# Kernel tuning notes

Hardware: AMD Instinct MI355X
Metric: run time of the kernel (lower is better)

The kernel has to match this reference:

```python
import jax, jax.numpy as jnp
import numpy as np

D_MODEL = 1024
N_HEADS = 16
D_K = D_MODEL // N_HEADS
THETA = 10000.0
SEQ = 2048
BATCH = 2


def setup_inputs() -> dict:
    key = jax.random.key(0)
    ks = jax.random.split(key, 5)
    std = (2.0 / (D_MODEL + D_MODEL)) ** 0.5
    return {
        "x": jax.random.normal(ks[0], (BATCH, SEQ, D_MODEL), dtype=jnp.float32),
        "token_positions": jnp.arange(SEQ, dtype=jnp.int64 if jax.config.jax_enable_x64 else jnp.int32),
        "wq": jax.random.normal(ks[1], (D_MODEL, D_MODEL), dtype=jnp.float32) * std,
        "wk": jax.random.normal(ks[2], (D_MODEL, D_MODEL), dtype=jnp.float32) * std,
        "wv": jax.random.normal(ks[3], (D_MODEL, D_MODEL), dtype=jnp.float32) * std,
        "wo": jax.random.normal(ks[4], (D_MODEL, D_MODEL), dtype=jnp.float32) * std,
    }


def _apply_rope(t, token_positions):
    # t: [b, h, s, d_k]; interleaved even/odd rotation (RoPE)
    k = jnp.arange(D_K // 2, dtype=t.dtype)
    inv_freq = THETA ** (-2.0 * k / D_K)                     # [d_k/2]
    angles = token_positions.astype(t.dtype)[:, None] * inv_freq  # [s, d_k/2]
    cos, sin = jnp.cos(angles), jnp.sin(angles)
    even, odd = t[..., 0::2], t[..., 1::2]
    re = even * cos - odd * sin
    ro = odd * cos + even * sin
    # re-interleave: stack last then reshape back to [..., d_k]
    return jnp.stack([re, ro], axis=-1).reshape(t.shape)


def reference(x, token_positions, wq, wk, wv, wo):
    b, s, _ = x.shape
    def proj(w):
        y = jnp.einsum("bsd,ed->bse", x, w)               # Linear: x @ W^T
        return y.reshape(b, s, N_HEADS, D_K).transpose(0, 2, 1, 3)  # [b,h,s,dk]
    q, k, v = proj(wq), proj(wk), proj(wv)
    q = _apply_rope(q, token_positions)
    k = _apply_rope(k, token_positions)
    scores = jnp.einsum("bhqd,bhkd->bhqk", q, k) / jnp.sqrt(jnp.asarray(D_K, x.dtype))
    attn = jax.nn.softmax(scores, axis=-1)
    out = jnp.einsum("bhqk,bhkd->bhqd", attn, v)          # [b,h,s,dk]
    out = out.transpose(0, 2, 1, 3).reshape(b, s, D_MODEL)
    return jnp.einsum("bsd,ed->bse", out, wo)
```

## Files before the change

kernel.cpp:

```cpp
#include <hip/hip_runtime.h>
#include <stdint.h>

typedef __bf16 bf16x8 __attribute__((ext_vector_type(8)));
typedef __bf16 bf16x2 __attribute__((ext_vector_type(2)));
typedef float f32x4 __attribute__((ext_vector_type(4)));
typedef unsigned short ushort_t;
typedef unsigned int uint;

#define SEQ    2048
#define DMODEL 1024
#define NHEAD  16
#define DKH    64
#define NBATCH 2
#define MROWS  (NBATCH*SEQ)
#define LOG2E  1.44269504088896340736f

__device__ __forceinline__ uint pk2(float a, float b) {
  bf16x2 t; t[0] = (__bf16)a; t[1] = (__bf16)b;
  return __builtin_bit_cast(uint, t);
}
__device__ __forceinline__ ushort_t b1(float a) {
  return __builtin_bit_cast(ushort_t, (__bf16)a);
}
__device__ __forceinline__ float fexp2(float x) {
#if __has_builtin(__builtin_amdgcn_exp2f)
  return __builtin_amdgcn_exp2f(x);
#else
  return exp2f(x);
#endif
}

__device__ __forceinline__ void gload16(const void* g, void* l) {
  __builtin_amdgcn_global_load_lds(
      (const __attribute__((address_space(1))) void*)g,
      (__attribute__((address_space(3))) void*)l, 16, 0, 0);
}

__device__ __forceinline__ f32x4 mfma16(bf16x8 a, bf16x8 b, f32x4 c) {
  return __builtin_amdgcn_mfma_f32_16x16x32_bf16(a, b, c, 0, 0, 0);
}

__global__ __launch_bounds__(256) void cvt_all(
    const float* __restrict__ x, const float* __restrict__ wq,
    const float* __restrict__ wk, const float* __restrict__ wv,
    const float* __restrict__ wo, uint2* __restrict__ out)
{
  int b = blockIdx.x;
  const float4* src; uint2* dst; int i;
  if (b < 4096) {
    i = b * 256 + threadIdx.x; src = (const float4*)x; dst = out;
  } else {
    int s = (b - 4096) >> 10;
    i = ((b - 4096) & 1023) * 256 + threadIdx.x;
    src = (const float4*)(s == 0 ? wq : s == 1 ? wk : s == 2 ? wv : wo);
    dst = out + (size_t)1048576 + (size_t)s * 262144;
  }
  float4 v = src[i];
  uint2 r; r.x = pk2(v.x, v.y); r.y = pk2(v.z, v.w);
  dst[i] = r;
}

__global__ __launch_bounds__(256) void rope_tab_kernel(const int* __restrict__ tokpos, float2* __restrict__ tab) {
  int t = blockIdx.x * 256 + threadIdx.x;
  int s = t >> 5, k = t & 31;
  double inv = pow(10000.0, -(double)(2 * k) / 64.0);
  double ang = (double)tokpos[s] * inv;
  tab[t] = make_float2((float)cos(ang), (float)sin(ang));
}

__global__ __launch_bounds__(256) void gemm_nt(
    const ushort_t* __restrict__ A, const ushort_t* __restrict__ W,
    const float2* __restrict__ tab,
    ushort_t* __restrict__ Qo, ushort_t* __restrict__ Ko, ushort_t* __restrict__ Vo,
    float* __restrict__ outf, int fused)
{
  __shared__ ushort_t lA[2][128 * 64];
  __shared__ ushort_t lB[2][128 * 64];
  const int tid = threadIdx.x;
  const int w = tid >> 6, l = tid & 63, lo = l & 15, hi = l >> 4;
  const int wr = (w >> 1) * 64, wc = (w & 1) * 64;
  const char* Ab = (const char*)A + (size_t)blockIdx.y * 128 * 2048;
  const char* Bb = (const char*)W + (size_t)blockIdx.x * 128 * 2048;
  f32x4 acc[4][4] = {};

  const int o0 = w * 1024 + l * 16;
  const int r0 = o0 >> 7;
  const int us = ((o0 >> 4) & 7) ^ (r0 & 7);
  const char* ap = Ab + (size_t)r0 * 2048 + us * 16;
  const char* bp = Bb + (size_t)r0 * 2048 + us * 16;

  auto stage = [&](char* dA, char* dB, const char* aq, const char* bq) {
    #pragma unroll
    for (int i = 0; i < 4; ++i) {
      gload16(aq + i * 65536, dA + w * 1024 + i * 4096);
      gload16(bq + i * 65536, dB + w * 1024 + i * 4096);
    }
  };
  auto comp = [&](const ushort_t* lAb, const ushort_t* lBb) {
    #pragma unroll
    for (int c = 0; c < 2; ++c) {
      bf16x8 af[4], wf[4];
      #pragma unroll
      for (int m = 0; m < 4; ++m) {
        int row = wr + m * 16 + lo;
        af[m] = *(const bf16x8*)((const char*)lAb + row * 128 + ((c * 64 + hi * 16) ^ ((row & 7) << 4)));
      }
      #pragma unroll
      for (int n = 0; n < 4; ++n) {
        int row = wc + n * 16 + lo;
        wf[n] = *(const bf16x8*)((const char*)lBb + row * 128 + ((c * 64 + hi * 16) ^ ((row & 7) << 4)));
      }
      #pragma unroll
      for (int m = 0; m < 4; ++m)
        #pragma unroll
        for (int n = 0; n < 4; ++n)
          acc[m][n] = mfma16(af[m], wf[n], acc[m][n]);
    }
  };

  stage((char*)lA[0], (char*)lB[0], ap, bp); ap += 128; bp += 128;
  __syncthreads();
  for (int it = 0; it < 16; it += 2) {
    stage((char*)lA[1], (char*)lB[1], ap, bp); ap += 128; bp += 128;
    comp(lA[0], lB[0]);
    __syncthreads();
    if (it + 2 < 16) { stage((char*)lA[0], (char*)lB[0], ap, bp); ap += 128; bp += 128; }
    comp(lA[1], lB[1]);
    __syncthreads();
  }

  const int mode = fused ? (blockIdx.x >> 3) : 3;
  const int colblk = fused ? (blockIdx.x & 7) : blockIdx.x;
  const int rowbase = blockIdx.y * 128 + wr + hi * 4;
  const int colbase = colblk * 128 + wc + lo;

  if (mode == 3) {
    #pragma unroll
    for (int m = 0; m < 4; ++m)
      #pragma unroll
      for (int n = 0; n < 4; ++n) {
        int e = colbase + n * 16;
        #pragma unroll
        for (int r = 0; r < 4; ++r) {
          int row = rowbase + m * 16 + r;
          outf[(size_t)row * 1024 + e] = acc[m][n][r];
        }
      }
    return;
  }
  if (mode == 2) {
    #pragma unroll
    for (int m = 0; m < 4; ++m) {
      int row0 = rowbase + m * 16;
      int b = row0 >> 11, s = row0 & 2047;
      #pragma unroll
      for (int n = 0; n < 4; ++n) {
        int e = colbase + n * 16;
        int h = e >> 6, dk = e & 63;
        uint2 pk;
        pk.x = pk2(acc[m][n][0], acc[m][n][1]);
        pk.y = pk2(acc[m][n][2], acc[m][n][3]);
        *(uint2*)(Vo + ((size_t)((b * NHEAD + h) * DKH + dk) * SEQ + s)) = pk;
      }
    }
    return;
  }
  ushort_t* outb = (mode == 0) ? Qo : Ko;
  const float qscale = (mode == 0) ? (0.125f * LOG2E) : 1.0f;
  #pragma unroll
  for (int m = 0; m < 4; ++m) {
    #pragma unroll
    for (int n = 0; n < 4; ++n) {
      int e = colbase + n * 16;
      int h = e >> 6, dk = e & 63, kf = dk >> 1;
      float sgn = (e & 1) ? 1.0f : -1.0f;
      #pragma unroll
      for (int r = 0; r < 4; ++r) {
        int row = rowbase + m * 16 + r;
        int s = row & 2047, b = row >> 11;
        float2 cs = tab[s * 32 + kf];
        float v = acc[m][n][r];
        float p = __shfl_xor(v, 1, 64);
        float res = (v * cs.x + sgn * p * cs.y) * qscale;
        outb[((size_t)((b * NHEAD + h) * SEQ + s)) * DKH + dk] = b1(res);
      }
    }
  }
}

__global__ __launch_bounds__(256) void attn_fwd(
    const ushort_t* __restrict__ Qg, const ushort_t* __restrict__ Kg,
    const ushort_t* __restrict__ VTg, ushort_t* __restrict__ attn)
{
  __shared__ ushort_t lK[2][64 * 64];
  __shared__ ushort_t lVT[2][64 * 64];
  __shared__ ushort_t lP[4][16 * 64];
  const int tid = threadIdx.x;
  const int w = tid >> 6, l = tid & 63, lo = l & 15, hi = l >> 4;
  const int bh = blockIdx.y;
  const int q0 = blockIdx.x * 64 + w * 16;
  const char* Kb = (const char*)Kg + (size_t)bh * 2048 * 128;
  const char* Vb = (const char*)VTg + (size_t)bh * 64 * 4096;

  bf16x8 qreg[2];
  {
    const ushort_t* qp = Qg + ((size_t)bh * 2048 + q0 + lo) * 64 + hi * 8;
    qreg[0] = *(const bf16x8*)qp;
    qreg[1] = *(const bf16x8*)(qp + 32);
  }

  f32x4 accO[4] = {};
  float lsum = 0.f;

  const int o0 = w * 1024 + l * 16;
  const int r0 = o0 >> 7;
  const int us = ((o0 >> 4) & 7) ^ (r0 & 7);
  const char* kp = Kb + (size_t)r0 * 128 + us * 16;
  const char* vp = Vb + (size_t)r0 * 4096 + us * 16;

  auto stage = [&](char* dK, char* dV, const char* kq, const char* vq) {
    gload16(kq,          dK + w * 1024);
    gload16(kq + 4096,   dK + w * 1024 + 4096);
    gload16(vq,          dV + w * 1024);
    gload16(vq + 131072, dV + w * 1024 + 4096);
  };

  auto qkpv = [&](const ushort_t* lKb, const ushort_t* lVb) {
    f32x4 s4[4];
    #pragma unroll
    for (int g = 0; g < 4; ++g) {
      int row = g * 16 + lo;
      const char* base = (const char*)lKb + row * 128;
      int sw = (row & 7) << 4;
      bf16x8 k0 = *(const bf16x8*)(base + ((hi * 16) ^ sw));
      bf16x8 k1 = *(const bf16x8*)(base + ((64 + hi * 16) ^ sw));
      s4[g] = mfma16(k0, qreg[0], (f32x4){0.f, 0.f, 0.f, 0.f});
      s4[g] = mfma16(k1, qreg[1], s4[g]);
    }
    float ts = 0.f;
    float p[4][4];
    #pragma unroll
    for (int g = 0; g < 4; ++g)
      #pragma unroll
      for (int r = 0; r < 4; ++r) {
        p[g][r] = fexp2(s4[g][r]);
        ts += p[g][r];
      }
    lsum += ts;

    #pragma unroll
    for (int g = 0; g < 4; ++g) {
      uint2 pk;
      pk.x = pk2(p[g][0], p[g][1]);
      pk.y = pk2(p[g][2], p[g][3]);
      *(uint2*)((char*)lP[w] + lo * 128 + ((g * 32 + hi * 8) ^ ((lo & 7) << 4))) = pk;
    }
    int swp = (lo & 7) << 4;
    bf16x8 pf0 = *(const bf16x8*)((const char*)lP[w] + lo * 128 + ((hi * 16) ^ swp));
    bf16x8 pf1 = *(const bf16x8*)((const char*)lP[w] + lo * 128 + ((64 + hi * 16) ^ swp));

    #pragma unroll
    for (int gd = 0; gd < 4; ++gd) {
      int row = gd * 16 + lo;
      const char* vb = (const char*)lVb + row * 128;
      int sw = (row & 7) << 4;
      bf16x8 v0 = *(const bf16x8*)(vb + ((hi * 16) ^ sw));
      bf16x8 v1 = *(const bf16x8*)(vb + ((64 + hi * 16) ^ sw));
      accO[gd] = mfma16(v0, pf0, accO[gd]);
      accO[gd] = mfma16(v1, pf1, accO[gd]);
    }
  };

  stage((char*)lK[0], (char*)lVT[0], kp, vp); kp += 8192; vp += 128;
  for (int kt = 0; kt < 32; kt += 2) {
    __syncthreads();
    stage((char*)lK[1], (char*)lVT[1], kp, vp); kp += 8192; vp += 128;
    qkpv(lK[0], lVT[0]);
    __syncthreads();
    if (kt + 2 < 32) { stage((char*)lK[0], (char*)lVT[0], kp, vp); kp += 8192; vp += 128; }
    qkpv(lK[1], lVT[1]);
  }

  float lt = lsum;
  lt += __shfl_xor(lt, 16, 64);
  lt += __shfl_xor(lt, 32, 64);
  float inv = 1.0f / lt;
  int b = bh >> 4, hH = bh & 15;
  int rowg = (b << 11) + q0 + lo;
  #pragma unroll
  for (int gd = 0; gd < 4; ++gd) {
    uint2 pk;
    pk.x = pk2(accO[gd][0] * inv, accO[gd][1] * inv);
    pk.y = pk2(accO[gd][2] * inv, accO[gd][3] * inv);
    *(uint2*)(attn + (size_t)rowg * 1024 + hH * 64 + gd * 16 + hi * 4) = pk;
  }
}

extern "C" void kernel_launch(void* const* d_in, const int* in_sizes, int n_in,
                              void* d_out, int out_size, void* d_ws, size_t ws_size,
                              hipStream_t stream) {
  const float* x  = (const float*)d_in[0];
  const int* tok  = (const int*)d_in[1];
  const float* wq = (const float*)d_in[2];
  const float* wk = (const float*)d_in[3];
  const float* wv = (const float*)d_in[4];
  const float* wo = (const float*)d_in[5];
  float* out = (float*)d_out;
  char* ws = (char*)d_ws;

  size_t off = 0;
  float2* tab = (float2*)(ws + off); off += (size_t)SEQ * 32 * sizeof(float2);
  ushort_t* xb  = (ushort_t*)(ws + off); off += (size_t)MROWS * DMODEL * 2;
  ushort_t* wqkv = (ushort_t*)(ws + off); off += (size_t)3 * DMODEL * DMODEL * 2;
  ushort_t* wob = (ushort_t*)(ws + off); off += (size_t)DMODEL * DMODEL * 2;
  ushort_t* Qg  = (ushort_t*)(ws + off); off += (size_t)MROWS * DMODEL * 2;
  ushort_t* Kg  = (ushort_t*)(ws + off); off += (size_t)MROWS * DMODEL * 2;
  ushort_t* VTg = (ushort_t*)(ws + off); off += (size_t)MROWS * DMODEL * 2;
  ushort_t* attnb = xb;
  if (ws_size < off) return;

  cvt_all<<<8192, 256, 0, stream>>>(x, wq, wk, wv, wo, (uint2*)xb);
  rope_tab_kernel<<<256, 256, 0, stream>>>(tok, tab);

  gemm_nt<<<dim3(24, 32), 256, 0, stream>>>(xb, wqkv, tab, Qg, Kg, VTg, nullptr, 1);

  attn_fwd<<<dim3(SEQ / 64, NBATCH * NHEAD), 256, 0, stream>>>(Qg, Kg, VTg, attnb);

  gemm_nt<<<dim3(8, 32), 256, 0, stream>>>(attnb, wob, nullptr, nullptr, nullptr, nullptr, out, 0);
}
```

Before: 136.3 us.

## Switch attention to 32x32x16 MFMA with 128-query blocks per workgroup

Rewrites the attention kernel so each wave handles 32 query rows using 32x32x16 bf16 MFMA instead of 16x16x32. Each workgroup now covers 128 queries, halving the grid and reusing each staged K/V tile across twice as many queries. This cuts global K/V traffic and LDS reads per FLOP. The cost is higher register pressure from 16-wide accumulators and fewer workgroups (512) to fill the GPU.

```diff
diff --git a/kernel.cpp b/kernel.cpp
--- a/kernel.cpp
+++ b/kernel.cpp
@@ -4,6 +4,7 @@
 typedef __bf16 bf16x8 __attribute__((ext_vector_type(8)));
 typedef __bf16 bf16x2 __attribute__((ext_vector_type(2)));
 typedef float f32x4 __attribute__((ext_vector_type(4)));
+typedef float f32x16 __attribute__((ext_vector_type(16)));
 typedef unsigned short ushort_t;
 typedef unsigned int uint;
 
@@ -38,6 +39,9 @@
 
 __device__ __forceinline__ f32x4 mfma16(bf16x8 a, bf16x8 b, f32x4 c) {
   return __builtin_amdgcn_mfma_f32_16x16x32_bf16(a, b, c, 0, 0, 0);
+}
+__device__ __forceinline__ f32x16 mfma32(bf16x8 a, bf16x8 b, f32x16 c) {
+  return __builtin_amdgcn_mfma_f32_32x32x16_bf16(a, b, c, 0, 0, 0);
 }
 
 __global__ __launch_bounds__(256) void cvt_all(
@@ -192,108 +196,104 @@
     const ushort_t* __restrict__ Qg, const ushort_t* __restrict__ Kg,
     const ushort_t* __restrict__ VTg, ushort_t* __restrict__ attn)
 {
-  __shared__ ushort_t lK[2][64 * 64];
-  __shared__ ushort_t lVT[2][64 * 64];
-  __shared__ ushort_t lP[4][16 * 64];
+  __shared__ char lds[49152];
   const int tid = threadIdx.x;
-  const int w = tid >> 6, l = tid & 63, lo = l & 15, hi = l >> 4;
+  const int w = tid >> 6, l = tid & 63;
+  const int q31 = l & 31, hf = l >> 5, s7 = l & 7;
   const int bh = blockIdx.y;
-  const int q0 = blockIdx.x * 64 + w * 16;
+  const int q0 = blockIdx.x * 128 + w * 32;
   const char* Kb = (const char*)Kg + (size_t)bh * 2048 * 128;
   const char* Vb = (const char*)VTg + (size_t)bh * 64 * 4096;
 
-  bf16x8 qreg[2];
+  bf16x8 qreg[4];
   {
-    const ushort_t* qp = Qg + ((size_t)bh * 2048 + q0 + lo) * 64 + hi * 8;
-    qreg[0] = *(const bf16x8*)qp;
-    qreg[1] = *(const bf16x8*)(qp + 32);
-  }
-
-  f32x4 accO[4] = {};
+    const ushort_t* qp = Qg + ((size_t)bh * 2048 + q0 + q31) * 64 + hf * 8;
+    #pragma unroll
+    for (int c = 0; c < 4; ++c) qreg[c] = *(const bf16x8*)(qp + c * 16);
+  }
+
+  f32x16 accO[2] = {{0,0,0,0,0,0,0,0,0,0,0,0,0,0,0,0},
+                    {0,0,0,0,0,0,0,0,0,0,0,0,0,0,0,0}};
   float lsum = 0.f;
 
-  const int o0 = w * 1024 + l * 16;
+  const char* ra[4];
+  #pragma unroll
+  for (int c = 0; c < 4; ++c)
+    ra[c] = lds + q31 * 128 + ((c * 32 + hf * 16) ^ (s7 << 4));
+  const int lPoff = 32768 + w * 4096;
+  char* wbase = lds + lPoff + q31 * 128 + hf * 8;
+
+  const int o0 = tid * 16;
   const int r0 = o0 >> 7;
   const int us = ((o0 >> 4) & 7) ^ (r0 & 7);
   const char* kp = Kb + (size_t)r0 * 128 + us * 16;
   const char* vp = Vb + (size_t)r0 * 4096 + us * 16;
 
-  auto stage = [&](char* dK, char* dV, const char* kq, const char* vq) {
-    gload16(kq,          dK + w * 1024);
-    gload16(kq + 4096,   dK + w * 1024 + 4096);
-    gload16(vq,          dV + w * 1024);
-    gload16(vq + 131072, dV + w * 1024 + 4096);
+  auto stage = [&](char* base, const char* kq, const char* vq) {
+    gload16(kq,          base + o0);
+    gload16(kq + 4096,   base + 4096 + o0);
+    gload16(vq,          base + 8192 + o0);
+    gload16(vq + 131072, base + 12288 + o0);
   };
 
-  auto qkpv = [&](const ushort_t* lKb, const ushort_t* lVb) {
-    f32x4 s4[4];
-    #pragma unroll
-    for (int g = 0; g < 4; ++g) {
-      int row = g * 16 + lo;
-      const char* base = (const char*)lKb + row * 128;
-      int sw = (row & 7) << 4;
-      bf16x8 k0 = *(const bf16x8*)(base + ((hi * 16) ^ sw));
-      bf16x8 k1 = *(const bf16x8*)(base + ((64 + hi * 16) ^ sw));
-      s4[g] = mfma16(k0, qreg[0], (f32x4){0.f, 0.f, 0.f, 0.f});
-      s4[g] = mfma16(k1, qreg[1], s4[g]);
-    }
-    float ts = 0.f;
-    float p[4][4];
-    #pragma unroll
-    for (int g = 0; g < 4; ++g)
-      #pragma unroll
-      for (int r = 0; r < 4; ++r) {
-        p[g][r] = fexp2(s4[g][r]);
-        ts += p[g][r];
-      }
-    lsum += ts;
-
-    #pragma unroll
-    for (int g = 0; g < 4; ++g) {
-      uint2 pk;
-      pk.x = pk2(p[g][0], p[g][1]);
-      pk.y = pk2(p[g][2], p[g][3]);
-      *(uint2*)((char*)lP[w] + lo * 128 + ((g * 32 + hi * 8) ^ ((lo & 7) << 4))) = pk;
-    }
-    int swp = (lo & 7) << 4;
-    bf16x8 pf0 = *(const bf16x8*)((const char*)lP[w] + lo * 128 + ((hi * 16) ^ swp));
-    bf16x8 pf1 = *(const bf16x8*)((const char*)lP[w] + lo * 128 + ((64 + hi * 16) ^ swp));
-
-    #pragma unroll
-    for (int gd = 0; gd < 4; ++gd) {
-      int row = gd * 16 + lo;
-      const char* vb = (const char*)lVb + row * 128;
-      int sw = (row & 7) << 4;
-      bf16x8 v0 = *(const bf16x8*)(vb + ((hi * 16) ^ sw));
-      bf16x8 v1 = *(const bf16x8*)(vb + ((64 + hi * 16) ^ sw));
-      accO[gd] = mfma16(v0, pf0, accO[gd]);
-      accO[gd] = mfma16(v1, pf1, accO[gd]);
+  auto tile = [&](int bo) {
+    #pragma unroll
+    for (int kb = 0; kb < 2; ++kb) {
+      f32x16 s = {0,0,0,0,0,0,0,0,0,0,0,0,0,0,0,0};
+      #pragma unroll
+      for (int c = 0; c < 4; ++c) {
+        bf16x8 kf = *(const bf16x8*)(ra[c] + bo + kb * 4096);
+        s = mfma32(kf, qreg[c], s);
+      }
+      float p[16];
+      float ts = 0.f;
+      #pragma unroll
+      for (int r = 0; r < 16; ++r) { p[r] = fexp2(s[r]); ts += p[r]; }
+      lsum += ts;
+      #pragma unroll
+      for (int g2 = 0; g2 < 4; ++g2) {
+        uint2 pk;
+        pk.x = pk2(p[g2 * 4 + 0], p[g2 * 4 + 1]);
+        pk.y = pk2(p[g2 * 4 + 2], p[g2 * 4 + 3]);
+        *(uint2*)(wbase + ((kb * 64 + g2 * 16) ^ (s7 << 4))) = pk;
+      }
+      #pragma unroll
+      for (int kcl = 0; kcl < 2; ++kcl) {
+        int kc = kb * 2 + kcl;
+        bf16x8 pb = *(const bf16x8*)(ra[kc] + lPoff);
+        #pragma unroll
+        for (int db = 0; db < 2; ++db) {
+          bf16x8 vf = *(const bf16x8*)(ra[kc] + bo + 8192 + db * 4096);
+          accO[db] = mfma32(vf, pb, accO[db]);
+        }
+      }
     }
   };
 
-  stage((char*)lK[0], (char*)lVT[0], kp, vp); kp += 8192; vp += 128;
+  stage(lds, kp, vp); kp += 8192; vp += 128;
   for (int kt = 0; kt < 32; kt += 2) {
     __syncthreads();
-    stage((char*)lK[1], (char*)lVT[1], kp, vp); kp += 8192; vp += 128;
-    qkpv(lK[0], lVT[0]);
+    stage(lds + 16384, kp, vp); kp += 8192; vp += 128;
+    tile(0);
     __syncthreads();
-    if (kt + 2 < 32) { stage((char*)lK[0], (char*)lVT[0], kp, vp); kp += 8192; vp += 128; }
-    qkpv(lK[1], lVT[1]);
-  }
-
-  float lt = lsum;
-  lt += __shfl_xor(lt, 16, 64);
-  lt += __shfl_xor(lt, 32, 64);
+    if (kt + 2 < 32) { stage(lds, kp, vp); kp += 8192; vp += 128; }
+    tile(16384);
+  }
+
+  float lt = lsum + __shfl_xor(lsum, 32, 64);
   float inv = 1.0f / lt;
-  int b = bh >> 4, hH = bh & 15;
-  int rowg = (b << 11) + q0 + lo;
+  int b = bh >> 4, head = bh & 15;
+  ushort_t* op = attn + (size_t)(b * 2048 + q0 + q31) * 1024 + head * 64;
   #pragma unroll
-  for (int gd = 0; gd < 4; ++gd) {
-    uint2 pk;
-    pk.x = pk2(accO[gd][0] * inv, accO[gd][1] * inv);
-    pk.y = pk2(accO[gd][2] * inv, accO[gd][3] * inv);
-    *(uint2*)(attn + (size_t)rowg * 1024 + hH * 64 + gd * 16 + hi * 4) = pk;
-  }
+  for (int db = 0; db < 2; ++db)
+    #pragma unroll
+    for (int m = 0; m < 4; ++m) {
+      int d0 = db * 32 + m * 8 + hf * 4;
+      uint2 pk;
+      pk.x = pk2(accO[db][m * 4 + 0] * inv, accO[db][m * 4 + 1] * inv);
+      pk.y = pk2(accO[db][m * 4 + 2] * inv, accO[db][m * 4 + 3] * inv);
+      *(uint2*)(op + d0) = pk;
+    }
 }
 
 extern "C" void kernel_launch(void* const* d_in, const int* in_sizes, int n_in,
@@ -324,7 +324,7 @@
 
   gemm_nt<<<dim3(24, 32), 256, 0, stream>>>(xb, wqkv, tab, Qg, Kg, VTg, nullptr, 1);
 
-  attn_fwd<<<dim3(SEQ / 64, NBATCH * NHEAD), 256, 0, stream>>>(Qg, Kg, VTg, attnb);
+  attn_fwd<<<dim3(SEQ / 128, NBATCH * NHEAD), 256, 0, stream>>>(Qg, Kg, VTg, attnb);
 
   gemm_nt<<<dim3(8, 32), 256, 0, stream>>>(attnb, wob, nullptr, nullptr, nullptr, nullptr, out, 0);
 }
```

After: 131.9 us. 1.03x faster.
